# Optimization experiments

Measured on AMD Instinct MI355X. Metric: run time of the kernel, lower is better.

## Reference

```python
import jax, jax.numpy as jnp
import numpy as np

EMBED_DIM = 1024
HEAD_DIM = 64


def setup_inputs() -> dict:
    key = jax.random.key(0)
    ks = jax.random.split(key, 7)
    B, S = 4, 2048
    s = 1.0 / np.sqrt(EMBED_DIM)
    h = jax.random.normal(ks[0], (B, S, EMBED_DIM), dtype=jnp.float32)
    Wq = jax.random.normal(ks[1], (EMBED_DIM, HEAD_DIM), dtype=jnp.float32) * s
    bq = jax.random.normal(ks[2], (HEAD_DIM,), dtype=jnp.float32) * 0.01
    Wk = jax.random.normal(ks[3], (EMBED_DIM, HEAD_DIM), dtype=jnp.float32) * s
    bk = jax.random.normal(ks[4], (HEAD_DIM,), dtype=jnp.float32) * 0.01
    Wv = jax.random.normal(ks[5], (EMBED_DIM, HEAD_DIM), dtype=jnp.float32) * s
    bv = jax.random.normal(ks[6], (HEAD_DIM,), dtype=jnp.float32) * 0.01
    return {"h": h, "Wq": Wq, "bq": bq, "Wk": Wk, "bk": bk, "Wv": Wv, "bv": bv}


def reference(h, Wq, bq, Wk, bk, Wv, bv):
    # Linear projections: h [B,S,E] -> q,k [B,S,D]
    q = jnp.einsum("bse,ed->bsd", h, Wq) + bq
    k = jnp.einsum("bse,ed->bsd", h, Wk) + bk
    v = jnp.einsum("bse,ed->bsd", h, Wv) + bv  # computed but UNUSED (faithful to source)
    del v
    scale = 1.0 / jnp.sqrt(jnp.asarray(HEAD_DIM, dtype=q.dtype))
    # scores [B, Sq, Sk]
    scores = jnp.einsum("bqd,bkd->bqk", q, k) * scale
    # NOTE: source uses softmax over dim=1 (query axis), not the key axis
    weights = jax.nn.softmax(scores, axis=1)
    # NOTE: source passes h (not v) as the value tensor
    out = jnp.einsum("bqk,bke->bqe", weights, h)  # [B, Sq, E]
    return out
```

## Files before the change

kernel.cpp:

```cpp
#include <hip/hip_runtime.h>
#include <hip/hip_bf16.h>
#include <math.h>

#define EMBED 1024
#define HDIM  64
#define BATCH 4
#define SEQ   2048

typedef __attribute__((ext_vector_type(8))) short short8;
typedef __attribute__((ext_vector_type(4))) float f32x4;
typedef unsigned int u32;
typedef unsigned short u16;

static __device__ __forceinline__ u16 f2bf(float f) {
    union { float f; u32 u; } v; v.f = f;
    u32 r = v.u + 0x7fffu + ((v.u >> 16) & 1u);
    return (u16)(r >> 16);
}

static __device__ __forceinline__ void gload_lds16(const u16* g, u16* l) {
    __builtin_amdgcn_global_load_lds(
        (const __attribute__((address_space(1))) u32*)g,
        (__attribute__((address_space(3))) u32*)l, 16, 0, 0);
}

__global__ __launch_bounds__(256) void wt_kernel(
    const float* __restrict__ Wq, const float* __restrict__ Wk,
    u16* __restrict__ WqT, u16* __restrict__ WkT)
{
    __shared__ float tile[64][65];
    const float* W = blockIdx.y ? Wk : Wq;
    u16* WT = blockIdx.y ? WkT : WqT;
    int e0 = blockIdx.x * 64;
    int t = threadIdx.x, c = t & 63, r4 = t >> 6;
    for (int r = r4; r < 64; r += 4)
        tile[r][c] = W[(size_t)(e0 + r) * HDIM + c];
    __syncthreads();
    for (int d = r4; d < 64; d += 4)
        WT[(size_t)d * EMBED + e0 + c] = f2bf(tile[c][d]);
}

__global__ __launch_bounds__(256) void proj_kernel(
    const float* __restrict__ h, const u16* __restrict__ WqT, const u16* __restrict__ WkT,
    const float* __restrict__ bq, const float* __restrict__ bk,
    u16* __restrict__ Qbf, u16* __restrict__ Kbf)
{
    __shared__ u16 hs[2][16][136];
    int b = blockIdx.x >> 7, s0 = (blockIdx.x & 127) * 16;
    int t = threadIdx.x, lane = t & 63, w = t >> 6;
    int l15 = lane & 15, quad = lane >> 4;
    int pj = w >> 1, nh = (w & 1) * 32;
    const float* hb = h + ((size_t)b * SEQ + s0) * EMBED;
    const u16* Wp = pj ? WkT : WqT;
    int r = t >> 4, c4 = (t & 15) * 4;

    f32x4 preA0 = *(const f32x4*)(hb + (size_t)r * EMBED + c4);
    f32x4 preA1 = *(const f32x4*)(hb + (size_t)r * EMBED + 64 + c4);
    f32x4 preB0 = *(const f32x4*)(hb + (size_t)r * EMBED + 128 + c4);
    f32x4 preB1 = *(const f32x4*)(hb + (size_t)r * EMBED + 192 + c4);
    f32x4 accA[2], accB[2];
    accA[0] = accA[1] = accB[0] = accB[1] = (f32x4){0.f, 0.f, 0.f, 0.f};

    const u16* Wrow0 = Wp + (size_t)(nh + l15) * EMBED;
    const u16* Wrow1 = Wp + (size_t)(nh + 16 + l15) * EMBED;

    short8 cw[8];
#pragma unroll
    for (int i = 0; i < 4; i++) {
        cw[i]     = *(const short8*)(Wrow0 + i * 32 + quad * 8);
        cw[4 + i] = *(const short8*)(Wrow1 + i * 32 + quad * 8);
    }

    for (int it = 0; it < 8; ++it) {
        int ec = it * 128, buf = it & 1;
        uint2 pk;
        pk.x = (u32)f2bf(preA0[0]) | ((u32)f2bf(preA0[1]) << 16);
        pk.y = (u32)f2bf(preA0[2]) | ((u32)f2bf(preA0[3]) << 16);
        *(uint2*)&hs[buf][r][c4] = pk;
        pk.x = (u32)f2bf(preA1[0]) | ((u32)f2bf(preA1[1]) << 16);
        pk.y = (u32)f2bf(preA1[2]) | ((u32)f2bf(preA1[3]) << 16);
        *(uint2*)&hs[buf][r][64 + c4] = pk;
        __syncthreads();

        preA0 = preB0; preA1 = preB1;
        if (it + 2 < 8) {
            preB0 = *(const f32x4*)(hb + (size_t)r * EMBED + ec + 256 + c4);
            preB1 = *(const f32x4*)(hb + (size_t)r * EMBED + ec + 320 + c4);
        }
        short8 nw[8];
#pragma unroll
        for (int i = 0; i < 8; i++) nw[i] = cw[i];
        if (it + 1 < 8) {
#pragma unroll
            for (int i = 0; i < 4; i++) {
                nw[i]     = *(const short8*)(Wrow0 + ec + 128 + i * 32 + quad * 8);
                nw[4 + i] = *(const short8*)(Wrow1 + ec + 128 + i * 32 + quad * 8);
            }
        }

        short8 a0 = *(const short8*)&hs[buf][l15][quad * 8];
        short8 a1 = *(const short8*)&hs[buf][l15][32 + quad * 8];
        short8 a2 = *(const short8*)&hs[buf][l15][64 + quad * 8];
        short8 a3 = *(const short8*)&hs[buf][l15][96 + quad * 8];
        accA[0] = __builtin_amdgcn_mfma_f32_16x16x32_bf16(a0, cw[0], accA[0], 0, 0, 0);
        accA[1] = __builtin_amdgcn_mfma_f32_16x16x32_bf16(a0, cw[4], accA[1], 0, 0, 0);
        accB[0] = __builtin_amdgcn_mfma_f32_16x16x32_bf16(a1, cw[1], accB[0], 0, 0, 0);
        accB[1] = __builtin_amdgcn_mfma_f32_16x16x32_bf16(a1, cw[5], accB[1], 0, 0, 0);
        accA[0] = __builtin_amdgcn_mfma_f32_16x16x32_bf16(a2, cw[2], accA[0], 0, 0, 0);
        accA[1] = __builtin_amdgcn_mfma_f32_16x16x32_bf16(a2, cw[6], accA[1], 0, 0, 0);
        accB[0] = __builtin_amdgcn_mfma_f32_16x16x32_bf16(a3, cw[3], accB[0], 0, 0, 0);
        accB[1] = __builtin_amdgcn_mfma_f32_16x16x32_bf16(a3, cw[7], accB[1], 0, 0, 0);
#pragma unroll
        for (int i = 0; i < 8; i++) cw[i] = nw[i];
    }

    const float* bias = pj ? bk : bq;
    float scale = pj ? 1.0f : 0.125f;
    u16* outp = pj ? Kbf : Qbf;
    float bv0 = bias[nh + l15], bv1 = bias[nh + 16 + l15];
#pragma unroll
    for (int rr = 0; rr < 4; rr++) {
        size_t row = (size_t)b * SEQ + s0 + quad * 4 + rr;
        outp[row * HDIM + nh + l15]      = f2bf((accA[0][rr] + accB[0][rr] + bv0) * scale);
        outp[row * HDIM + nh + 16 + l15] = f2bf((accA[1][rr] + accB[1][rr] + bv1) * scale);
    }
}

__global__ __launch_bounds__(256) void sw_kernel(
    const u16* __restrict__ Qbf, const u16* __restrict__ Kbf,
    u16* __restrict__ Wmat, float* __restrict__ invl)
{
    __shared__ float sl[4][16];
    int b = blockIdx.y;
    int k0 = blockIdx.x * 16;
    int t = threadIdx.x, lane = t & 63, w = t >> 6;
    int l15 = lane & 15, quad = lane >> 4;
    const u16* Qb = Qbf + (size_t)b * SEQ * HDIM;
    const u16* Kb = Kbf + (size_t)b * SEQ * HDIM;
    u16* Wb = Wmat + (size_t)b * SEQ * SEQ;
    short8 kf0 = *(const short8*)(Kb + (size_t)(k0 + l15) * HDIM + quad * 8);
    short8 kf1 = *(const short8*)(Kb + (size_t)(k0 + l15) * HDIM + 32 + quad * 8);
    f32x4 lacc = {0.f, 0.f, 0.f, 0.f};
    int qs = w * 512;
    const u16* qpa = Qb + (size_t)(qs + l15) * HDIM;
    const u16* qpb = Qb + (size_t)(qs + 16 + l15) * HDIM;
    short8 cf0a = *(const short8*)(qpa + quad * 8);
    short8 cf1a = *(const short8*)(qpa + 32 + quad * 8);
    short8 cf0b = *(const short8*)(qpb + quad * 8);
    short8 cf1b = *(const short8*)(qpb + 32 + quad * 8);

    for (int q0 = qs; q0 < qs + 512; q0 += 32) {
        short8 nf0a = cf0a, nf1a = cf1a, nf0b = cf0b, nf1b = cf1b;
        if (q0 + 32 < qs + 512) {
            const u16* na = Qb + (size_t)(q0 + 32 + l15) * HDIM;
            const u16* nb = Qb + (size_t)(q0 + 48 + l15) * HDIM;
            nf0a = *(const short8*)(na + quad * 8);
            nf1a = *(const short8*)(na + 32 + quad * 8);
            nf0b = *(const short8*)(nb + quad * 8);
            nf1b = *(const short8*)(nb + 32 + quad * 8);
        }
        f32x4 aa = {0.f, 0.f, 0.f, 0.f}, ab = {0.f, 0.f, 0.f, 0.f};
        aa = __builtin_amdgcn_mfma_f32_16x16x32_bf16(kf0, cf0a, aa, 0, 0, 0);
        ab = __builtin_amdgcn_mfma_f32_16x16x32_bf16(kf0, cf0b, ab, 0, 0, 0);
        aa = __builtin_amdgcn_mfma_f32_16x16x32_bf16(kf1, cf1a, aa, 0, 0, 0);
        ab = __builtin_amdgcn_mfma_f32_16x16x32_bf16(kf1, cf1b, ab, 0, 0, 0);
        float e0 = __expf(aa[0]), e1 = __expf(aa[1]);
        float e2 = __expf(aa[2]), e3 = __expf(aa[3]);
        float g0 = __expf(ab[0]), g1 = __expf(ab[1]);
        float g2 = __expf(ab[2]), g3 = __expf(ab[3]);
        lacc[0] += e0 + g0; lacc[1] += e1 + g1;
        lacc[2] += e2 + g2; lacc[3] += e3 + g3;
        uint2 pa, pb;
        pa.x = (u32)f2bf(e0) | ((u32)f2bf(e1) << 16);
        pa.y = (u32)f2bf(e2) | ((u32)f2bf(e3) << 16);
        pb.x = (u32)f2bf(g0) | ((u32)f2bf(g1) << 16);
        pb.y = (u32)f2bf(g2) | ((u32)f2bf(g3) << 16);
        *(uint2*)(Wb + (size_t)(q0 + l15) * SEQ + k0 + quad * 4) = pa;
        *(uint2*)(Wb + (size_t)(q0 + 16 + l15) * SEQ + k0 + quad * 4) = pb;
        cf0a = nf0a; cf1a = nf1a; cf0b = nf0b; cf1b = nf1b;
    }
#pragma unroll
    for (int m = 1; m <= 8; m <<= 1) {
        lacc[0] += __shfl_xor(lacc[0], m, 64);
        lacc[1] += __shfl_xor(lacc[1], m, 64);
        lacc[2] += __shfl_xor(lacc[2], m, 64);
        lacc[3] += __shfl_xor(lacc[3], m, 64);
    }
    if (l15 == 0) {
        sl[w][quad * 4 + 0] = lacc[0];
        sl[w][quad * 4 + 1] = lacc[1];
        sl[w][quad * 4 + 2] = lacc[2];
        sl[w][quad * 4 + 3] = lacc[3];
    }
    __syncthreads();
    if (t < 16)
        invl[b * SEQ + k0 + t] =
            1.0f / ((sl[0][t] + sl[1][t]) + (sl[2][t] + sl[3][t]));
}

__global__ __launch_bounds__(256) void tscale_kernel(
    const float* __restrict__ h, const float* __restrict__ invl,
    u16* __restrict__ hT)
{
    __shared__ float tile[64][65];
    int b  = blockIdx.z;
    int s0 = blockIdx.x * 64, e0 = blockIdx.y * 64;
    int t = threadIdx.x;
    int r16 = t >> 4, c4 = (t & 15) * 4;
    const float* hb = h + (size_t)b * SEQ * EMBED;
#pragma unroll
    for (int rr = r16; rr < 64; rr += 16) {
        f32x4 v = *(const f32x4*)(hb + (size_t)(s0 + rr) * EMBED + e0 + c4);
        *(f32x4*)&tile[rr][c4] = v;
    }
    __syncthreads();
    f32x4 il4 = *(const f32x4*)(invl + b * SEQ + s0 + c4);
    u16* hTb = hT + (size_t)b * EMBED * SEQ;
#pragma unroll
    for (int er = r16; er < 64; er += 16) {
        u16 p0 = f2bf(tile[c4 + 0][er] * il4[0]);
        u16 p1 = f2bf(tile[c4 + 1][er] * il4[1]);
        u16 p2 = f2bf(tile[c4 + 2][er] * il4[2]);
        u16 p3 = f2bf(tile[c4 + 3][er] * il4[3]);
        uint2 pk;
        pk.x = (u32)p0 | ((u32)p1 << 16);
        pk.y = (u32)p2 | ((u32)p3 << 16);
        *(uint2*)(hTb + (size_t)(e0 + er) * SEQ + s0 + c4) = pk;
    }
}

__global__ __launch_bounds__(512, 2) void out_gemm_kernel(
    const u16* __restrict__ Wmat, const u16* __restrict__ hT, float* __restrict__ out)
{
    __shared__ __align__(16) char smem[3 * 49152];
    int b = blockIdx.z;
    int q0 = blockIdx.x * 256, e0 = blockIdx.y * 128;
    int t = threadIdx.x, lane = t & 63, w = t >> 6;
    int l15 = lane & 15, quad = lane >> 4;
    const u16* Wb  = Wmat + (size_t)b * SEQ * SEQ;
    const u16* hTb = hT + (size_t)b * EMBED * SEQ;
    int kf = w >> 2;
    int wm = (w >> 1) & 1, wn = w & 1;
    int wq = wm * 128, we = wn * 64;

    f32x4 acc[8][4];
#pragma unroll
    for (int i = 0; i < 8; i++)
#pragma unroll
        for (int j = 0; j < 4; j++) acc[i][j] = (f32x4){0.f, 0.f, 0.f, 0.f};

    int st_rl = lane >> 3;
    int st_pc = lane & 7;

    const u16* gA[4];
    const u16* gB[2];
#pragma unroll
    for (int ld = 0; ld < 4; ld++) {
        int row = w * 32 + ld * 8 + st_rl;
        int cg  = st_pc ^ (row & 7);
        gA[ld] = Wb + (size_t)(q0 + row) * SEQ + cg * 8;
    }
#pragma unroll
    for (int ld = 0; ld < 2; ld++) {
        int row = w * 16 + ld * 8 + st_rl;
        int cg  = st_pc ^ (row & 7);
        gB[ld] = hTb + (size_t)(e0 + row) * SEQ + cg * 8;
    }
    int dA[4], dB[2];
#pragma unroll
    for (int ld = 0; ld < 4; ld++) dA[ld] = (w * 32 + ld * 8) * 128 + lane * 16;
#pragma unroll
    for (int ld = 0; ld < 2; ld++) dB[ld] = 32768 + (w * 16 + ld * 8) * 128 + lane * 16;
    int offA[8], offB[4];
#pragma unroll
    for (int ii = 0; ii < 8; ii++) {
        int ra  = wq + ii * 16 + l15;
        int pca = (kf * 4 + quad) ^ (ra & 7);
        offA[ii] = ra * 128 + pca * 16;
    }
#pragma unroll
    for (int j = 0; j < 4; j++) {
        int rb  = we + j * 16 + l15;
        int pcb = (kf * 4 + quad) ^ (rb & 7);
        offB[j] = 32768 + rb * 128 + pcb * 16;
    }

#define STAGE_H1(si)                                                           \
    {                                                                          \
        gload_lds16(gA[0], (u16*)(smem + (si) * 49152 + dA[0]));               \
        gload_lds16(gA[1], (u16*)(smem + (si) * 49152 + dA[1]));               \
        gload_lds16(gB[0], (u16*)(smem + (si) * 49152 + dB[0]));               \
    }
#define STAGE_H2(si)                                                           \
    {                                                                          \
        gload_lds16(gA[2], (u16*)(smem + (si) * 49152 + dA[2]));               \
        gload_lds16(gA[3], (u16*)(smem + (si) * 49152 + dA[3]));               \
        gload_lds16(gB[1], (u16*)(smem + (si) * 49152 + dB[1]));               \
    }
#define ADV()                                                                  \
    {                                                                          \
        gA[0] += 64; gA[1] += 64; gA[2] += 64; gA[3] += 64;                    \
        gB[0] += 64; gB[1] += 64;                                              \
    }

#define MFMA16(i0)                                                             \
    {                                                                          \
        _Pragma("unroll")                                                      \
        for (int ii = 0; ii < 4; ii++)                                         \
            _Pragma("unroll")                                                  \
            for (int j = 0; j < 4; j++)                                        \
                acc[(i0) + ii][j] = __builtin_amdgcn_mfma_f32_16x16x32_bf16(   \
                    af[ii], bfr[j], acc[(i0) + ii][j], 0, 0, 0);               \
    }

#define TILE(si, si2, DO_STAGE, VMC)                                           \
    {                                                                          \
        const char* Sb = smem + (si) * 49152;                                  \
        short8 af[4], bfr[4];                                                  \
        _Pragma("unroll")                                                      \
        for (int ii = 0; ii < 4; ii++)                                         \
            af[ii] = *(const short8*)(Sb + offA[ii]);                          \
        _Pragma("unroll")                                                      \
        for (int j = 0; j < 4; j++)                                            \
            bfr[j] = *(const short8*)(Sb + offB[j]);                           \
        if (DO_STAGE) STAGE_H1(si2)                                            \
        __builtin_amdgcn_s_setprio(1);                                         \
        MFMA16(0)                                                              \
        __builtin_amdgcn_s_setprio(0);                                         \
        _Pragma("unroll")                                                      \
        for (int ii = 0; ii < 4; ii++)                                         \
            af[ii] = *(const short8*)(Sb + offA[4 + ii]);                      \
        if (DO_STAGE) { STAGE_H2(si2) ADV() }                                  \
        __builtin_amdgcn_s_setprio(1);                                         \
        MFMA16(4)                                                              \
        __builtin_amdgcn_s_setprio(0);                                         \
        if ((VMC) == 6) { asm volatile("s_waitcnt vmcnt(6)" ::: "memory"); }   \
        else if ((VMC) == 0) { asm volatile("s_waitcnt vmcnt(0)" ::: "memory"); } \
        __builtin_amdgcn_s_barrier();                                          \
    }

    STAGE_H1(0) STAGE_H2(0) ADV()
    STAGE_H1(1) STAGE_H2(1) ADV()
    asm volatile("s_waitcnt vmcnt(6)" ::: "memory");
    __builtin_amdgcn_s_barrier();

    for (int g = 0; g < 10; ++g) {
        TILE(0, 2, true, 6)
        TILE(1, 0, true, 6)
        TILE(2, 1, true, 6)
    }
    TILE(0, 2, false, 0)
    TILE(1, 0, false, -1)
#undef TILE
#undef STAGE_H1
#undef STAGE_H2
#undef ADV
#undef MFMA16

    float* red = (float*)smem;
    if (w >= 4) {
        float* reg = red + (size_t)(w & 3) * 8192;
#pragma unroll
        for (int i = 0; i < 8; i++)
#pragma unroll
            for (int j = 0; j < 4; j++)
                *(f32x4*)(reg + ((i * 4 + j) * 64 + lane) * 4) = acc[i][j];
    }
    __syncthreads();
    if (w < 4) {
        float* reg = red + (size_t)w * 8192;
        float* outb = out + (size_t)b * SEQ * EMBED;
#pragma unroll
        for (int i = 0; i < 8; i++)
#pragma unroll
            for (int j = 0; j < 4; j++) {
                f32x4 o = *(const f32x4*)(reg + ((i * 4 + j) * 64 + lane) * 4);
                o += acc[i][j];
#pragma unroll
                for (int r = 0; r < 4; r++)
                    outb[(size_t)(q0 + wq + i * 16 + quad * 4 + r) * EMBED
                         + e0 + we + j * 16 + l15] = o[r];
            }
    }
}

extern "C" void kernel_launch(void* const* d_in, const int* in_sizes, int n_in,
                              void* d_out, int out_size, void* d_ws, size_t ws_size,
                              hipStream_t stream) {
    (void)in_sizes; (void)n_in; (void)out_size; (void)ws_size;
    const float* h  = (const float*)d_in[0];
    const float* Wq = (const float*)d_in[1];
    const float* bq = (const float*)d_in[2];
    const float* Wk = (const float*)d_in[3];
    const float* bk = (const float*)d_in[4];
    float* out = (float*)d_out;

    char* ws = (char*)d_ws;
    u16*   Qbf  = (u16*)(ws);
    u16*   Kbf  = (u16*)(ws + (1ull << 20));
    u16*   hT   = (u16*)(ws + (2ull << 20));
    float* invl = (float*)(ws + (18ull << 20));
    u16*   WqT  = (u16*)(ws + (18ull << 20) + (128ull << 10));
    u16*   WkT  = (u16*)(ws + (18ull << 20) + (256ull << 10));
    u16*   Wmat = (u16*)(ws + (19ull << 20));

    hipLaunchKernelGGL(wt_kernel, dim3(16, 2), dim3(256), 0, stream, Wq, Wk, WqT, WkT);
    hipLaunchKernelGGL(proj_kernel, dim3(512), dim3(256), 0, stream,
                       h, WqT, WkT, bq, bk, Qbf, Kbf);
    hipLaunchKernelGGL(sw_kernel, dim3(128, 4), dim3(256), 0, stream,
                       Qbf, Kbf, Wmat, invl);
    hipLaunchKernelGGL(tscale_kernel, dim3(32, 16, 4), dim3(256), 0, stream,
                       h, invl, hT);
    hipLaunchKernelGGL(out_gemm_kernel, dim3(8, 8, 4), dim3(512), 0, stream,
                       Wmat, hT, out);
}
```

Before: 173.9 us.

## Widen score kernel to 64 keys per block and add barrier-synced MFMA phases

The score/exp kernel now has each block handle 64 key columns with 512 threads. Each wave holds four K fragments and covers 256 queries, so every Q fragment load feeds eight MFMAs instead of two. Writes to the weight matrix become 128-byte contiguous rows per query instead of 32-byte ones, which should improve store coalescing. The output GEMM tile loop gains extra workgroup barriers, lgkmcnt waits and scheduling barriers around its MFMA groups to interleave the waves. This adds sync overhead and cuts the sw_kernel grid from 512 to 128 blocks, which may underfill the GPU.

```diff
diff --git a/kernel.cpp b/kernel.cpp
--- a/kernel.cpp
+++ b/kernel.cpp
@@ -126,76 +126,112 @@
     }
 }
 
-__global__ __launch_bounds__(256) void sw_kernel(
+__global__ __launch_bounds__(512) void sw_kernel(
     const u16* __restrict__ Qbf, const u16* __restrict__ Kbf,
     u16* __restrict__ Wmat, float* __restrict__ invl)
 {
-    __shared__ float sl[4][16];
+    __shared__ float sl[8][64];
     int b = blockIdx.y;
-    int k0 = blockIdx.x * 16;
+    int k0 = blockIdx.x * 64;
     int t = threadIdx.x, lane = t & 63, w = t >> 6;
     int l15 = lane & 15, quad = lane >> 4;
     const u16* Qb = Qbf + (size_t)b * SEQ * HDIM;
     const u16* Kb = Kbf + (size_t)b * SEQ * HDIM;
     u16* Wb = Wmat + (size_t)b * SEQ * SEQ;
-    short8 kf0 = *(const short8*)(Kb + (size_t)(k0 + l15) * HDIM + quad * 8);
-    short8 kf1 = *(const short8*)(Kb + (size_t)(k0 + l15) * HDIM + 32 + quad * 8);
-    f32x4 lacc = {0.f, 0.f, 0.f, 0.f};
-    int qs = w * 512;
-    const u16* qpa = Qb + (size_t)(qs + l15) * HDIM;
-    const u16* qpb = Qb + (size_t)(qs + 16 + l15) * HDIM;
-    short8 cf0a = *(const short8*)(qpa + quad * 8);
-    short8 cf1a = *(const short8*)(qpa + 32 + quad * 8);
-    short8 cf0b = *(const short8*)(qpb + quad * 8);
-    short8 cf1b = *(const short8*)(qpb + 32 + quad * 8);
-
-    for (int q0 = qs; q0 < qs + 512; q0 += 32) {
-        short8 nf0a = cf0a, nf1a = cf1a, nf0b = cf0b, nf1b = cf1b;
-        if (q0 + 32 < qs + 512) {
-            const u16* na = Qb + (size_t)(q0 + 32 + l15) * HDIM;
-            const u16* nb = Qb + (size_t)(q0 + 48 + l15) * HDIM;
-            nf0a = *(const short8*)(na + quad * 8);
-            nf1a = *(const short8*)(na + 32 + quad * 8);
-            nf0b = *(const short8*)(nb + quad * 8);
-            nf1b = *(const short8*)(nb + 32 + quad * 8);
-        }
-        f32x4 aa = {0.f, 0.f, 0.f, 0.f}, ab = {0.f, 0.f, 0.f, 0.f};
-        aa = __builtin_amdgcn_mfma_f32_16x16x32_bf16(kf0, cf0a, aa, 0, 0, 0);
-        ab = __builtin_amdgcn_mfma_f32_16x16x32_bf16(kf0, cf0b, ab, 0, 0, 0);
-        aa = __builtin_amdgcn_mfma_f32_16x16x32_bf16(kf1, cf1a, aa, 0, 0, 0);
-        ab = __builtin_amdgcn_mfma_f32_16x16x32_bf16(kf1, cf1b, ab, 0, 0, 0);
-        float e0 = __expf(aa[0]), e1 = __expf(aa[1]);
-        float e2 = __expf(aa[2]), e3 = __expf(aa[3]);
-        float g0 = __expf(ab[0]), g1 = __expf(ab[1]);
-        float g2 = __expf(ab[2]), g3 = __expf(ab[3]);
-        lacc[0] += e0 + g0; lacc[1] += e1 + g1;
-        lacc[2] += e2 + g2; lacc[3] += e3 + g3;
-        uint2 pa, pb;
-        pa.x = (u32)f2bf(e0) | ((u32)f2bf(e1) << 16);
-        pa.y = (u32)f2bf(e2) | ((u32)f2bf(e3) << 16);
-        pb.x = (u32)f2bf(g0) | ((u32)f2bf(g1) << 16);
-        pb.y = (u32)f2bf(g2) | ((u32)f2bf(g3) << 16);
-        *(uint2*)(Wb + (size_t)(q0 + l15) * SEQ + k0 + quad * 4) = pa;
-        *(uint2*)(Wb + (size_t)(q0 + 16 + l15) * SEQ + k0 + quad * 4) = pb;
-        cf0a = nf0a; cf1a = nf1a; cf0b = nf0b; cf1b = nf1b;
-    }
-#pragma unroll
-    for (int m = 1; m <= 8; m <<= 1) {
-        lacc[0] += __shfl_xor(lacc[0], m, 64);
-        lacc[1] += __shfl_xor(lacc[1], m, 64);
-        lacc[2] += __shfl_xor(lacc[2], m, 64);
-        lacc[3] += __shfl_xor(lacc[3], m, 64);
-    }
+
+    short8 kfr[4][2];
+#pragma unroll
+    for (int g = 0; g < 4; g++)
+#pragma unroll
+        for (int hh = 0; hh < 2; hh++)
+            kfr[g][hh] = *(const short8*)(
+                Kb + (size_t)(k0 + g * 16 + l15) * HDIM + hh * 32 + quad * 8);
+
+    f32x4 lacc[4];
+#pragma unroll
+    for (int g = 0; g < 4; g++) lacc[g] = (f32x4){0.f, 0.f, 0.f, 0.f};
+
+    int qs = w * 256;
+    short8 cf[2][2];
+#pragma unroll
+    for (int a = 0; a < 2; a++)
+#pragma unroll
+        for (int hh = 0; hh < 2; hh++)
+            cf[a][hh] = *(const short8*)(
+                Qb + (size_t)(qs + a * 16 + l15) * HDIM + hh * 32 + quad * 8);
+
+    for (int q0 = qs; q0 < qs + 256; q0 += 32) {
+        short8 nf[2][2];
+#pragma unroll
+        for (int a = 0; a < 2; a++)
+#pragma unroll
+            for (int hh = 0; hh < 2; hh++) nf[a][hh] = cf[a][hh];
+        if (q0 + 32 < qs + 256) {
+#pragma unroll
+            for (int a = 0; a < 2; a++)
+#pragma unroll
+                for (int hh = 0; hh < 2; hh++)
+                    nf[a][hh] = *(const short8*)(
+                        Qb + (size_t)(q0 + 32 + a * 16 + l15) * HDIM + hh * 32 + quad * 8);
+        }
+        f32x4 acc[2][4];
+#pragma unroll
+        for (int a = 0; a < 2; a++)
+#pragma unroll
+            for (int g = 0; g < 4; g++) acc[a][g] = (f32x4){0.f, 0.f, 0.f, 0.f};
+#pragma unroll
+        for (int a = 0; a < 2; a++)
+#pragma unroll
+            for (int g = 0; g < 4; g++) {
+                acc[a][g] = __builtin_amdgcn_mfma_f32_16x16x32_bf16(
+                    kfr[g][0], cf[a][0], acc[a][g], 0, 0, 0);
+                acc[a][g] = __builtin_amdgcn_mfma_f32_16x16x32_bf16(
+                    kfr[g][1], cf[a][1], acc[a][g], 0, 0, 0);
+            }
+#pragma unroll
+        for (int a = 0; a < 2; a++) {
+            u16* wrow = Wb + (size_t)(q0 + a * 16 + l15) * SEQ + k0;
+#pragma unroll
+            for (int g = 0; g < 4; g++) {
+                float e0 = __expf(acc[a][g][0]), e1 = __expf(acc[a][g][1]);
+                float e2 = __expf(acc[a][g][2]), e3 = __expf(acc[a][g][3]);
+                lacc[g][0] += e0; lacc[g][1] += e1;
+                lacc[g][2] += e2; lacc[g][3] += e3;
+                uint2 pk;
+                pk.x = (u32)f2bf(e0) | ((u32)f2bf(e1) << 16);
+                pk.y = (u32)f2bf(e2) | ((u32)f2bf(e3) << 16);
+                *(uint2*)(wrow + g * 16 + quad * 4) = pk;
+            }
+        }
+#pragma unroll
+        for (int a = 0; a < 2; a++)
+#pragma unroll
+            for (int hh = 0; hh < 2; hh++) cf[a][hh] = nf[a][hh];
+    }
+#pragma unroll
+    for (int m = 1; m <= 8; m <<= 1)
+#pragma unroll
+        for (int g = 0; g < 4; g++) {
+            lacc[g][0] += __shfl_xor(lacc[g][0], m, 64);
+            lacc[g][1] += __shfl_xor(lacc[g][1], m, 64);
+            lacc[g][2] += __shfl_xor(lacc[g][2], m, 64);
+            lacc[g][3] += __shfl_xor(lacc[g][3], m, 64);
+        }
     if (l15 == 0) {
-        sl[w][quad * 4 + 0] = lacc[0];
-        sl[w][quad * 4 + 1] = lacc[1];
-        sl[w][quad * 4 + 2] = lacc[2];
-        sl[w][quad * 4 + 3] = lacc[3];
+#pragma unroll
+        for (int g = 0; g < 4; g++) {
+            sl[w][g * 16 + quad * 4 + 0] = lacc[g][0];
+            sl[w][g * 16 + quad * 4 + 1] = lacc[g][1];
+            sl[w][g * 16 + quad * 4 + 2] = lacc[g][2];
+            sl[w][g * 16 + quad * 4 + 3] = lacc[g][3];
+        }
     }
     __syncthreads();
-    if (t < 16)
-        invl[b * SEQ + k0 + t] =
-            1.0f / ((sl[0][t] + sl[1][t]) + (sl[2][t] + sl[3][t]));
+    if (t < 64) {
+        float s = ((sl[0][t] + sl[1][t]) + (sl[2][t] + sl[3][t]))
+                + ((sl[4][t] + sl[5][t]) + (sl[6][t] + sl[7][t]));
+        invl[b * SEQ + k0 + t] = 1.0f / s;
+    }
 }
 
 __global__ __launch_bounds__(256) void tscale_kernel(
@@ -317,6 +353,7 @@
     {                                                                          \
         const char* Sb = smem + (si) * 49152;                                  \
         short8 af[4], bfr[4];                                                  \
+                                                                  \
         _Pragma("unroll")                                                      \
         for (int ii = 0; ii < 4; ii++)                                         \
             af[ii] = *(const short8*)(Sb + offA[ii]);                          \
@@ -324,13 +361,21 @@
         for (int j = 0; j < 4; j++)                                            \
             bfr[j] = *(const short8*)(Sb + offB[j]);                           \
         if (DO_STAGE) STAGE_H1(si2)                                            \
+        __builtin_amdgcn_s_barrier();                                          \
+        asm volatile("s_waitcnt lgkmcnt(0)" ::: "memory");                     \
+        __builtin_amdgcn_sched_barrier(0);                                     \
         __builtin_amdgcn_s_setprio(1);                                         \
         MFMA16(0)                                                              \
         __builtin_amdgcn_s_setprio(0);                                         \
+        __builtin_amdgcn_s_barrier();                                          \
+                                                                  \
         _Pragma("unroll")                                                      \
         for (int ii = 0; ii < 4; ii++)                                         \
             af[ii] = *(const short8*)(Sb + offA[4 + ii]);                      \
         if (DO_STAGE) { STAGE_H2(si2) ADV() }                                  \
+        __builtin_amdgcn_s_barrier();                                          \
+        asm volatile("s_waitcnt lgkmcnt(0)" ::: "memory");                     \
+        __builtin_amdgcn_sched_barrier(0);                                     \
         __builtin_amdgcn_s_setprio(1);                                         \
         MFMA16(4)                                                              \
         __builtin_amdgcn_s_setprio(0);                                         \
@@ -407,7 +452,7 @@
     hipLaunchKernelGGL(wt_kernel, dim3(16, 2), dim3(256), 0, stream, Wq, Wk, WqT, WkT);
     hipLaunchKernelGGL(proj_kernel, dim3(512), dim3(256), 0, stream,
                        h, WqT, WkT, bq, bk, Qbf, Kbf);
-    hipLaunchKernelGGL(sw_kernel, dim3(128, 4), dim3(256), 0, stream,
+    hipLaunchKernelGGL(sw_kernel, dim3(32, 4), dim3(512), 0, stream,
                        Qbf, Kbf, Wmat, invl);
     hipLaunchKernelGGL(tscale_kernel, dim3(32, 16, 4), dim3(256), 0, stream,
                        h, invl, hT);
```

New measurement: 177.6 us. 2.1% more time.
